# Kernel optimization log

Measured on AMD Instinct MI355X. Metric: run time of the kernel, lower is better.

Reference implementation:

```python
import jax, jax.numpy as jnp
from jax import lax
import numpy as np

B, IN, J, S, F, O, C, KS = 8, 8, 8, 187, 64, 64, 67, 15


def _ln(x, eps=1e-5):
    m = jnp.mean(x, axis=-1, keepdims=True)
    v = jnp.mean((x - m) ** 2, axis=-1, keepdims=True)
    return (x - m) / jnp.sqrt(v + eps)


def setup_inputs() -> dict:
    key = jax.random.key(0)
    ks = jax.random.split(key, 8)
    x_in = jax.random.normal(ks[0], (B, IN, S, F), jnp.float32)
    proj_x_prev = jax.random.normal(ks[1], (B, IN, S, O), jnp.float32)
    lin = jnp.linspace(-1.0, 1.0, C, dtype=jnp.float32)
    spline_weights = jnp.broadcast_to(lin, (IN, J, C)) + 0.01 * jax.random.normal(ks[2], (IN, J, C), jnp.float32)
    tau = 0.1 * jax.random.normal(ks[3], (IN, J), jnp.float32) + 0.1
    temperature = jnp.asarray(1.0, jnp.float32)
    omiga = jnp.full((IN, J), 0.2, jnp.float32)
    W2 = jax.random.normal(ks[4], (J, F, O), jnp.float32) * (1.0 / np.sqrt(F))
    b_param = 0.02 * jax.random.normal(ks[5], (J, S, O), jnp.float32)
    ln_scale = jnp.ones((J, F), jnp.float32)
    ln_bias = jnp.zeros((J, F), jnp.float32)
    alpha = jnp.ones((J,), jnp.float32)
    beta = jnp.ones((J,), jnp.float32)
    theta = jnp.ones((J,), jnp.float32)
    gamma = jnp.ones((J,), jnp.float32)
    w3 = 0.1 * jax.random.normal(ks[6], (J, O, KS), jnp.float32)  # depthwise conv kernels
    return dict(x_in=x_in, proj_x_prev=proj_x_prev, spline_weights=spline_weights, tau=tau,
                temperature=temperature, omiga=omiga, W2=W2, b_param=b_param, ln_scale=ln_scale,
                ln_bias=ln_bias, alpha=alpha, beta=beta, theta=theta, gamma=gamma, w3=w3)


def reference(x_in, proj_x_prev, spline_weights, tau, temperature, omiga, W2, b_param,
              ln_scale, ln_bias, alpha, beta, theta, gamma, w3):
    b, in_n, seq, feat = x_in.shape
    out_n, nC = spline_weights.shape[1], spline_weights.shape[2]
    kk = w3.shape[-1]
    # --- cubic B-spline basis ---
    h = 2.0 / (nC - 1)
    grid = jnp.linspace(-1.0, 1.0, nC, dtype=x_in.dtype)
    max_val = jnp.max(jnp.abs(x_in)) + 1e-8
    xn = jnp.clip(x_in / max_val * 0.95, -0.99, 0.99)
    dist = jnp.abs(xn[..., None] - grid) / h  # [b,in,seq,feat,C]
    basis = jax.nn.relu(2.0 - dist) ** 3 / 6.0 - jax.nn.relu(1.0 - dist) ** 3 * (4.0 / 6.0)
    spline_mapping = jnp.einsum('bisfc,ijc->bijsf', basis, spline_weights)
    activated = spline_mapping + jnp.abs(omiga)[None, :, :, None, None] * x_in[:, :, None]
    # --- energy-threshold gating ---
    energies = jnp.mean(activated ** 2, axis=(-1, -2))  # [b,in,out]
    tau_a = jnp.abs(tau)[None]
    t_val = jnp.abs(temperature) * np.sqrt(seq / 256.0) + 1e-4
    sqrtE = jnp.sqrt(energies + 1e-8)
    mask = jax.nn.sigmoid((sqrtE - tau_a) / t_val)  # [b,in,out]
    mult = sqrtE / (tau_a + 1e-8)
    wp = proj_x_prev[:, :, None] * (mult * mask)[..., None, None]  # [b,in,out,seq,d]
    d = wp.shape[-1]
    mid = in_n // 2
    Kt = wp[:, 0::2].transpose(0, 2, 3, 1, 4).reshape(b, out_n, seq, mid * d)
    Qt = wp[:, 1::2].transpose(0, 2, 3, 1, 4).reshape(b, out_n, seq, mid * d)
    Kt, Qt = _ln(Kt), _ln(Qt)
    raw = jnp.einsum('bjse,bjte->bjst', Kt, Qt)
    W1 = jax.nn.softmax(raw / (np.sqrt(mid * d) * t_val), axis=-1)  # [b,out,seq,seq]
    combined = jnp.einsum('bijsf,bij->bjsf', activated, mask)  # [b,out,seq,feat]
    # --- SplineWeightLayer (vectorized over out_n) ---
    xln = _ln(combined) * ln_scale[None, :, None, :] + ln_bias[None, :, None, :]
    x_prime = jnp.einsum('bjsh,jho->bjso', xln, W2) + b_param[None]  # [b,out,seq,O]
    o = x_prime.shape[-1]
    xt = x_prime.transpose(0, 2, 1, 3).reshape(b, seq, out_n * o)
    ker = w3.transpose(2, 0, 1).reshape(kk, 1, out_n * o)
    w3f = lax.conv_general_dilated(xt, ker, (1,), [(kk // 2, kk // 2)],
                                   dimension_numbers=('NWC', 'WIO', 'NWC'),
                                   feature_group_count=out_n * o)
    w3f = w3f.reshape(b, seq, out_n, o).transpose(0, 2, 1, 3)
    eye = jnp.eye(seq, dtype=x_in.dtype)
    attn_kernel = jnp.abs(beta)[None, :, None, None] * W1 + jnp.abs(alpha)[None, :, None, None] * eye
    global_part = jnp.einsum('bjst,bjto->bjso', attn_kernel, x_prime)
    spatial = global_part + jnp.abs(theta)[None, :, None, None] * w3f
    out = spatial + gamma[None, :, None, None] * combined  # residual_proj is Identity (F==O)
    return out, x_prime
```

## Files before the change

### kernel.cpp

```cpp
#include <hip/hip_runtime.h>
#include <math.h>

#define B_N 8
#define IN_N 8
#define J_N 8
#define S_N 187
#define F_N 64
#define O_N 64
#define C_N 67
#define KS_N 15
#define SF_N (S_N * F_N)
#define SF4_N (SF_N / 4)
#define E_N 256
#define SQRT_SF 0.85467470f

#define NT_SPL 12
#define NCOMB 96
#define NKTQT 2992
#define NZERO 16
#define NRAW 576
#define NXPR 768
#define NMAXP 256
#define FRAG_BJ 49152

typedef __attribute__((ext_vector_type(8))) _Float16 half8;
typedef __attribute__((ext_vector_type(4))) _Float16 half4;
typedef __attribute__((ext_vector_type(4))) float floatx4;

__device__ __forceinline__ float wave_sum(float v) {
#pragma unroll
  for (int off = 32; off > 0; off >>= 1) v += __shfl_down(v, off, 64);
  return __shfl(v, 0, 64);
}
__device__ __forceinline__ float wave_max(float v) {
#pragma unroll
  for (int off = 32; off > 0; off >>= 1) v = fmaxf(v, __shfl_down(v, off, 64));
  return __shfl(v, 0, 64);
}
__device__ __forceinline__ float lane_bc(float v, int l) {
  return __int_as_float(__builtin_amdgcn_readlane(__float_as_int(v), l));
}
__device__ __forceinline__ float bspline(float d) {
  float t2 = fmaxf(2.f - d, 0.f);
  float t1 = fmaxf(1.f - d, 0.f);
  return t2 * t2 * t2 * (1.f / 6.f) - t1 * t1 * t1 * (4.f / 6.f);
}
__device__ __forceinline__ float get_inv095(const float* __restrict__ maxp) {
  int lane = threadIdx.x & 63;
  float m = 0.f;
#pragma unroll
  for (int k = 0; k < NMAXP / 64; k++) m = fmaxf(m, maxp[lane + k * 64]);
  return 0.95f / (wave_max(m) + 1e-8f);
}
__device__ __forceinline__ float gate_g(const float* __restrict__ esum_p, int bi, int j,
                                        const float* __restrict__ tau, float tv) {
  const float* p = esum_p + ((long)bi * 8 + j) * NT_SPL;
  float s = 0.f;
#pragma unroll
  for (int k = 0; k < NT_SPL; k++) s += p[k];
  float sE = sqrtf(s * (1.f / (float)SF_N) + 1e-8f);
  float ta = fabsf(tau[(bi & 7) * 8 + j]);
  return (sE / (ta + 1e-8f)) / (1.f + expf(-(sE - ta) / tv));
}

__global__ void k_maxabs(const float4* __restrict__ x, float* __restrict__ maxp, int n4) {
  __shared__ float red[4];
  int tid = blockIdx.x * 256 + threadIdx.x;
  float m = 0.f;
  for (int i = tid; i < n4; i += gridDim.x * 256) {
    float4 v = x[i];
    m = fmaxf(m, fmaxf(fmaxf(fabsf(v.x), fabsf(v.y)), fmaxf(fabsf(v.z), fabsf(v.w))));
  }
  m = wave_max(m);
  if ((threadIdx.x & 63) == 0) red[threadIdx.x >> 6] = m;
  __syncthreads();
  if (threadIdx.x == 0)
    maxp[blockIdx.x] = fmaxf(fmaxf(red[0], red[1]), fmaxf(red[2], red[3]));
}

__global__ void k_spline(const float4* __restrict__ x4, const float* __restrict__ sw,
                         const float* __restrict__ omiga, const float* __restrict__ maxp,
                         float4* __restrict__ act4, float* __restrict__ esum_p) {
  int tile = blockIdx.x, bi = blockIdx.y;
  int i = bi & 7;
  __shared__ float wl[J_N * C_N];
  __shared__ float aom[J_N];
  __shared__ float red[4 * J_N];
  for (int t = threadIdx.x; t < J_N * C_N; t += 256) wl[t] = sw[i * J_N * C_N + t];
  if (threadIdx.x < J_N) aom[threadIdx.x] = fabsf(omiga[i * J_N + threadIdx.x]);
  int lane = threadIdx.x & 63, wid = threadIdx.x >> 6;
  float inv = get_inv095(maxp);
  __syncthreads();
  int i4 = tile * 256 + threadIdx.x;
  float e[J_N] = {0, 0, 0, 0, 0, 0, 0, 0};
  if (i4 < SF4_N) {
    float4 xv = x4[(long)bi * SF4_N + i4];
    float xs[4] = {xv.x, xv.y, xv.z, xv.w};
    float4 av[J_N];
#pragma unroll
    for (int c = 0; c < 4; c++) {
      float x = xs[c];
      float xn = fminf(fmaxf(x * inv, -0.99f), 0.99f);
      float u = (xn + 1.f) * 33.f;
      int c0 = (int)floorf(u) - 1;
      float sm[J_N] = {0, 0, 0, 0, 0, 0, 0, 0};
#pragma unroll
      for (int kk = 0; kk < 4; kk++) {
        int cc = c0 + kk;
        if (cc >= 0 && cc < C_N) {
          float bas = bspline(fabsf(u - (float)cc));
#pragma unroll
          for (int j = 0; j < J_N; j++) sm[j] += bas * wl[j * C_N + cc];
        }
      }
#pragma unroll
      for (int j = 0; j < J_N; j++) {
        float a = sm[j] + aom[j] * x;
        (&av[j].x)[c] = a;
        e[j] += a * a;
      }
    }
#pragma unroll
    for (int j = 0; j < J_N; j++) act4[((long)(bi * 8 + j)) * SF4_N + i4] = av[j];
  }
#pragma unroll
  for (int j = 0; j < J_N; j++) {
    float v = e[j];
#pragma unroll
    for (int off = 32; off > 0; off >>= 1) v += __shfl_down(v, off, 64);
    if (lane == 0) red[wid * J_N + j] = v;
  }
  __syncthreads();
  if (threadIdx.x < J_N)
    esum_p[((long)bi * 8 + threadIdx.x) * NT_SPL + tile] =
        red[threadIdx.x] + red[8 + threadIdx.x] + red[16 + threadIdx.x] + red[24 + threadIdx.x];
}

__global__ void k_mid2(const float4* __restrict__ act4, const float* __restrict__ esum_p,
                       const float* __restrict__ tau, const float* __restrict__ temp,
                       const float* __restrict__ proj, float4* __restrict__ comb4,
                       _Float16* __restrict__ khi, _Float16* __restrict__ klo,
                       _Float16* __restrict__ qhi, _Float16* __restrict__ qlo) {
  __shared__ float mk[64];
  int lane = threadIdx.x & 63;
  if (blockIdx.x < NCOMB) {
    int b = blockIdx.x / NT_SPL, tile = blockIdx.x - b * NT_SPL;
    if (threadIdx.x < 64) {
      int i = threadIdx.x >> 3, j = threadIdx.x & 7;
      const float* p = esum_p + ((long)(b * 8 + i) * 8 + j) * NT_SPL;
      float s = 0.f;
#pragma unroll
      for (int k = 0; k < NT_SPL; k++) s += p[k];
      float sE = sqrtf(s * (1.f / (float)SF_N) + 1e-8f);
      float ta = fabsf(tau[i * 8 + j]);
      float tv = fabsf(temp[0]) * SQRT_SF + 1e-4f;
      mk[threadIdx.x] = 1.f / (1.f + expf(-(sE - ta) / tv));
    }
    __syncthreads();
    int i4 = tile * 256 + threadIdx.x;
    if (i4 < SF4_N) {
      float4 cb[J_N] = {};
#pragma unroll
      for (int i = 0; i < IN_N; i++) {
#pragma unroll
        for (int j = 0; j < J_N; j++) {
          float4 a = act4[((long)((b * 8 + i) * 8 + j)) * SF4_N + i4];
          float g = mk[i * 8 + j];
          cb[j].x += g * a.x; cb[j].y += g * a.y;
          cb[j].z += g * a.z; cb[j].w += g * a.w;
        }
      }
#pragma unroll
      for (int j = 0; j < J_N; j++) comb4[((long)(b * J_N + j)) * SF4_N + i4] = cb[j];
    }
  } else if (blockIdx.x < NCOMB + NKTQT) {
    int w = threadIdx.x >> 6;
    int gr = (blockIdx.x - NCOMB) * 4 + w;
    int bj = gr / S_N, s = gr - bj * S_N;
    int b = bj >> 3, j = bj & 7;
    int ig = lane >> 4;
    int f4 = (lane & 15) * 4;
    int iK = b * 8 + 2 * ig;
    int iQ = iK + 1;
    float tv = fabsf(temp[0]) * SQRT_SF + 1e-4f;
    float gK = gate_g(esum_p, iK, j, tau, tv);
    float gQ = gate_g(esum_p, iQ, j, tau, tv);
    float4 kr = *(const float4*)(proj + ((long)iK * S_N + s) * 64 + f4);
    float4 qr = *(const float4*)(proj + ((long)iQ * S_N + s) * 64 + f4);
    float kv[4] = {kr.x * gK, kr.y * gK, kr.z * gK, kr.w * gK};
    float qv[4] = {qr.x * gQ, qr.y * gQ, qr.z * gQ, qr.w * gQ};
    float mkv = wave_sum(kv[0] + kv[1] + kv[2] + kv[3]) * (1.f / 256.f);
    float mqv = wave_sum(qv[0] + qv[1] + qv[2] + qv[3]) * (1.f / 256.f);
    float vk = 0.f, vq = 0.f;
#pragma unroll
    for (int q = 0; q < 4; q++) {
      float dk = kv[q] - mkv; vk += dk * dk;
      float dq = qv[q] - mqv; vq += dq * dq;
    }
    vk = wave_sum(vk) * (1.f / 256.f);
    vq = wave_sum(vq) * (1.f / 256.f);
    float ik = 1.f / sqrtf(vk + 1e-5f);
    float iq = 1.f / sqrtf(vq + 1e-5f);
    half4 hk4, lk4, hq4, lq4;
#pragma unroll
    for (int q = 0; q < 4; q++) {
      float fk = (kv[q] - mkv) * ik;
      float fq = (qv[q] - mqv) * iq;
      _Float16 hk = (_Float16)fk;
      _Float16 hq = (_Float16)fq;
      hk4[q] = hk; lk4[q] = (_Float16)(fk - (float)hk);
      hq4[q] = hq; lq4[q] = (_Float16)(fq - (float)hq);
    }
    int stile = s >> 4, m16 = s & 15;
    long fo = ((long)bj * 12 + stile) * 4096 + (lane >> 3) * 512 +
              (((lane >> 1) & 3) * 16 + m16) * 8 + (lane & 1) * 4;
    *(half4*)(khi + fo) = hk4;
    *(half4*)(klo + fo) = lk4;
    *(half4*)(qhi + fo) = hq4;
    *(half4*)(qlo + fo) = lq4;
  } else {
    int zb = blockIdx.x - (NCOMB + NKTQT);
    float4 z = {0.f, 0.f, 0.f, 0.f};
    for (int t = zb * 256 + threadIdx.x; t < 10240; t += NZERO * 256) {
      int bj = t / 160, r = t - bj * 160;
      int ec = r / 20, rr = r - ec * 20;
      int quad = rr / 5, m16 = 11 + rr - quad * 5;
      long fo = ((long)bj * 12 + 11) * 4096 + ec * 512 + (quad * 16 + m16) * 8;
      *(float4*)(khi + fo) = z;
      *(float4*)(klo + fo) = z;
      *(float4*)(qhi + fo) = z;
      *(float4*)(qlo + fo) = z;
    }
  }
}

__global__ void k_gemm(const _Float16* __restrict__ khi, const _Float16* __restrict__ klo,
                       const _Float16* __restrict__ qhi, const _Float16* __restrict__ qlo,
                       const float* __restrict__ temp, float* __restrict__ w1,
                       const float* __restrict__ comb, const float* __restrict__ W2,
                       const float* __restrict__ bparam, const float* __restrict__ lns,
                       const float* __restrict__ lnb, float* __restrict__ xprime) {
  __shared__ float smem[64 * 64 + 128];
  int lane = threadIdx.x & 63;
  if (blockIdx.x < NRAW) {
    int idx = blockIdx.x;
    int st = idx % 3, tt = (idx / 3) % 3, bj = idx / 9;
    int wave = threadIdx.x >> 6;
    int quad = lane >> 4, m16 = lane & 15;
    long fb = (long)bj * FRAG_BJ + lane * 8;
    const _Float16* ah_p = khi + fb + (st * 4 + wave) * 4096;
    const _Float16* al_p = klo + fb + (st * 4 + wave) * 4096;
    const _Float16* bh_p = qhi + fb + tt * 4 * 4096;
    const _Float16* bl_p = qlo + fb + tt * 4 * 4096;
    floatx4 acc[4] = {};
    for (int ec = 0; ec < 8; ec++) {
      half8 ah = *(const half8*)(ah_p + ec * 512);
      half8 al = *(const half8*)(al_p + ec * 512);
#pragma unroll
      for (int n = 0; n < 4; n++) {
        half8 bh = *(const half8*)(bh_p + n * 4096 + ec * 512);
        half8 bl = *(const half8*)(bl_p + n * 4096 + ec * 512);
        acc[n] = __builtin_amdgcn_mfma_f32_16x16x32_f16(ah, bh, acc[n], 0, 0, 0);
        acc[n] = __builtin_amdgcn_mfma_f32_16x16x32_f16(al, bh, acc[n], 0, 0, 0);
        acc[n] = __builtin_amdgcn_mfma_f32_16x16x32_f16(ah, bl, acc[n], 0, 0, 0);
      }
    }
    float tv = fabsf(temp[0]) * SQRT_SF + 1e-4f;
    float scale = 1.f / (16.f * tv);
#pragma unroll
    for (int n = 0; n < 4; n++) {
      int t = tt * 64 + n * 16 + m16;
      if (t >= S_N) continue;
#pragma unroll
      for (int r = 0; r < 4; r++) {
        int s = st * 64 + wave * 16 + quad * 4 + r;
        if (s < S_N) w1[((long)bj * S_N + s) * S_N + t] = acc[n][r] * scale;
      }
    }
  } else {
    int q = blockIdx.x - NRAW;
    int tile = q % 12, bj = q / 12;
    int j = bj & 7;
    float* w2s = smem;
    float* lss = smem + 4096;
    float* lbs = smem + 4160;
    const float4* wg = (const float4*)(W2 + j * 4096);
    float4* ws4 = (float4*)w2s;
    for (int idx = threadIdx.x; idx < 1024; idx += 256) ws4[idx] = wg[idx];
    if (threadIdx.x < 64) {
      lss[threadIdx.x] = lns[j * 64 + threadIdx.x];
      lbs[threadIdx.x] = lnb[j * 64 + threadIdx.x];
    }
    __syncthreads();
    int w = threadIdx.x >> 6;
    int sbase = tile * 16 + w * 4;
    float xln[4], acc[4];
#pragma unroll
    for (int rr = 0; rr < 4; rr++) {
      int s = sbase + rr;
      int sc = (s < S_N) ? s : S_N - 1;
      float x = comb[((long)bj * S_N + sc) * 64 + lane];
      float m = wave_sum(x) * (1.f / 64.f);
      float d = x - m;
      float var = wave_sum(d * d) * (1.f / 64.f);
      xln[rr] = d / sqrtf(var + 1e-5f) * lss[lane] + lbs[lane];
      acc[rr] = bparam[(j * S_N + sc) * 64 + lane];
    }
#pragma unroll
    for (int h = 0; h < 64; h++) {
      float w2v = w2s[h * 64 + lane];
#pragma unroll
      for (int rr = 0; rr < 4; rr++) acc[rr] += lane_bc(xln[rr], h) * w2v;
    }
#pragma unroll
    for (int rr = 0; rr < 4; rr++) {
      int s = sbase + rr;
      if (s < S_N) xprime[((long)bj * S_N + s) * 64 + lane] = acc[rr];
    }
  }
}

__global__ void k_final(const float* __restrict__ xprime, const float* __restrict__ w1,
                        const float* __restrict__ comb, const float* __restrict__ w3,
                        const float* __restrict__ alpha, const float* __restrict__ beta,
                        const float* __restrict__ theta, const float* __restrict__ gamma,
                        float* __restrict__ out) {
  int tile = blockIdx.x, bj = blockIdx.y;
  int j = bj & 7;
  __shared__ float w1t[16 * 188];
  int s0 = tile * 16;
  for (int idx = threadIdx.x; idx < 16 * S_N; idx += 256) {
    int r = idx / S_N, t = idx - r * S_N;
    int srow = s0 + r;
    w1t[r * 188 + t] = (srow < S_N) ? w1[((long)bj * S_N + srow) * S_N + t] : 0.f;
  }
  __syncthreads();
  int w = threadIdx.x >> 6, o = threadIdx.x & 63;
#pragma unroll
  for (int rr = 0; rr < 4; rr++) {
    float* row = &w1t[(w * 4 + rr) * 188];
    float v[3];
    float m = -1e30f;
#pragma unroll
    for (int q = 0; q < 3; q++) {
      int t = o + q * 64;
      v[q] = (t < S_N) ? row[t] : -1e30f;
      m = fmaxf(m, v[q]);
    }
    m = wave_max(m);
    float ssum = 0.f;
#pragma unroll
    for (int q = 0; q < 3; q++) {
      int t = o + q * 64;
      float e = (t < S_N) ? expf(v[q] - m) : 0.f;
      v[q] = e;
      ssum += e;
    }
    ssum = wave_sum(ssum);
    float invs = 1.f / ssum;
#pragma unroll
    for (int q = 0; q < 3; q++) {
      int t = o + q * 64;
      if (t < S_N) row[t] = v[q] * invs;
    }
  }
  float w3c[KS_N];
#pragma unroll
  for (int k = 0; k < KS_N; k++) w3c[k] = w3[j * 64 * KS_N + o * KS_N + k];
  const float* xpg = xprime + (long)bj * (S_N * 64);
  float aa = fabsf(alpha[j]), ba = fabsf(beta[j]), ta = fabsf(theta[j]), gv = gamma[j];
  float acc[4] = {0.f, 0.f, 0.f, 0.f};
  for (int t = 0; t < 184; t += 4) {
    float x0 = xpg[t * 64 + o];
    float x1 = xpg[(t + 1) * 64 + o];
    float x2 = xpg[(t + 2) * 64 + o];
    float x3 = xpg[(t + 3) * 64 + o];
#pragma unroll
    for (int rr = 0; rr < 4; rr++) {
      float4 wv = *(const float4*)&w1t[(w * 4 + rr) * 188 + t];
      acc[rr] += wv.x * x0 + wv.y * x1 + wv.z * x2 + wv.w * x3;
    }
  }
#pragma unroll
  for (int t = 184; t < S_N; t++) {
    float xv = xpg[t * 64 + o];
#pragma unroll
    for (int rr = 0; rr < 4; rr++) acc[rr] += w1t[(w * 4 + rr) * 188 + t] * xv;
  }
#pragma unroll
  for (int rr = 0; rr < 4; rr++) {
    int s = s0 + w * 4 + rr;
    if (s >= S_N) continue;
    float conv = 0.f;
#pragma unroll
    for (int k = 0; k < KS_N; k++) {
      int si = s + k - 7;
      if (si >= 0 && si < S_N) conv += xpg[si * 64 + o] * w3c[k];
    }
    float res = ba * acc[rr] + aa * xpg[s * 64 + o] + ta * conv +
                gv * comb[((long)bj * S_N + s) * 64 + o];
    out[((long)bj * S_N + s) * 64 + o] = res;
  }
}

extern "C" void kernel_launch(void* const* d_in, const int* in_sizes, int n_in,
                              void* d_out, int out_size, void* d_ws, size_t ws_size,
                              hipStream_t stream) {
  const float* x_in   = (const float*)d_in[0];
  const float* proj   = (const float*)d_in[1];
  const float* sw     = (const float*)d_in[2];
  const float* tau    = (const float*)d_in[3];
  const float* temp   = (const float*)d_in[4];
  const float* omiga  = (const float*)d_in[5];
  const float* W2     = (const float*)d_in[6];
  const float* bparam = (const float*)d_in[7];
  const float* lns    = (const float*)d_in[8];
  const float* lnb    = (const float*)d_in[9];
  const float* alpha  = (const float*)d_in[10];
  const float* beta   = (const float*)d_in[11];
  const float* theta  = (const float*)d_in[12];
  const float* gamma  = (const float*)d_in[13];
  const float* w3     = (const float*)d_in[14];

  float* out = (float*)d_out;
  float* xprime = out + B_N * J_N * S_N * O_N;

  float* wsf = (float*)d_ws;
  float* maxp   = wsf;
  float* esum_p = wsf + 512;
  float* act    = wsf + 512 + 512 * NT_SPL;
  const long FR = (long)64 * FRAG_BJ;
  _Float16* khi = (_Float16*)(act + (long)64 * 8 * SF_N);
  _Float16* klo = khi + FR;
  _Float16* qhi = klo + FR;
  _Float16* qlo = qhi + FR;
  float* w1   = (float*)(qlo + FR);
  float* comb = w1 + (long)B_N * J_N * S_N * S_N;

  k_maxabs<<<NMAXP, 256, 0, stream>>>((const float4*)x_in, maxp, (B_N * IN_N * S_N * F_N) / 4);
  k_spline<<<dim3(NT_SPL, 64), 256, 0, stream>>>((const float4*)x_in, sw, omiga, maxp,
                                                 (float4*)act, esum_p);
  k_mid2<<<NCOMB + NKTQT + NZERO, 256, 0, stream>>>((const float4*)act, esum_p, tau, temp,
                                                    proj, (float4*)comb, khi, klo, qhi, qlo);
  k_gemm<<<NRAW + NXPR, 256, 0, stream>>>(khi, klo, qhi, qlo, temp, w1,
                                          comb, W2, bparam, lns, lnb, xprime);
  k_final<<<dim3(12, 64), 256, 0, stream>>>(xprime, w1, comb, w3, alpha, beta, theta, gamma, out);
}
```

Baseline: 165.3 us.

## Recompute spline activations in combine stage instead of storing intermediate tensor

The spline kernel now computes only per-(b,i,j) energy sums and no longer writes the large activation tensor. The combine blocks of the middle kernel re-evaluate the B-spline basis from x_in for all input channels, then apply the gate mask directly. This trades a large global write and read of intermediates for duplicated spline arithmetic and a larger shared weight table in every block of the middle kernel.

Measured after the change: 169.4 us. 2.5% more time.

```diff
diff --git a/kernel.cpp b/kernel.cpp
--- a/kernel.cpp
+++ b/kernel.cpp
@@ -11,7 +11,6 @@
 #define KS_N 15
 #define SF_N (S_N * F_N)
 #define SF4_N (SF_N / 4)
-#define E_N 256
 #define SQRT_SF 0.85467470f
 
 #define NT_SPL 12
@@ -78,9 +77,9 @@
     maxp[blockIdx.x] = fmaxf(fmaxf(red[0], red[1]), fmaxf(red[2], red[3]));
 }
 
-__global__ void k_spline(const float4* __restrict__ x4, const float* __restrict__ sw,
-                         const float* __restrict__ omiga, const float* __restrict__ maxp,
-                         float4* __restrict__ act4, float* __restrict__ esum_p) {
+__global__ void k_energy2(const float4* __restrict__ x4, const float* __restrict__ sw,
+                          const float* __restrict__ omiga, const float* __restrict__ maxp,
+                          float* __restrict__ esum_p) {
   int tile = blockIdx.x, bi = blockIdx.y;
   int i = bi & 7;
   __shared__ float wl[J_N * C_N];
@@ -96,7 +95,6 @@
   if (i4 < SF4_N) {
     float4 xv = x4[(long)bi * SF4_N + i4];
     float xs[4] = {xv.x, xv.y, xv.z, xv.w};
-    float4 av[J_N];
 #pragma unroll
     for (int c = 0; c < 4; c++) {
       float x = xs[c];
@@ -116,12 +114,9 @@
 #pragma unroll
       for (int j = 0; j < J_N; j++) {
         float a = sm[j] + aom[j] * x;
-        (&av[j].x)[c] = a;
         e[j] += a * a;
       }
     }
-#pragma unroll
-    for (int j = 0; j < J_N; j++) act4[((long)(bi * 8 + j)) * SF4_N + i4] = av[j];
   }
 #pragma unroll
   for (int j = 0; j < J_N; j++) {
@@ -136,17 +131,23 @@
         red[threadIdx.x] + red[8 + threadIdx.x] + red[16 + threadIdx.x] + red[24 + threadIdx.x];
 }
 
-__global__ void k_mid2(const float4* __restrict__ act4, const float* __restrict__ esum_p,
-                       const float* __restrict__ tau, const float* __restrict__ temp,
-                       const float* __restrict__ proj, float4* __restrict__ comb4,
+__global__ void k_mid3(const float4* __restrict__ x4, const float* __restrict__ sw,
+                       const float* __restrict__ omiga, const float* __restrict__ maxp,
+                       const float* __restrict__ esum_p, const float* __restrict__ tau,
+                       const float* __restrict__ temp, const float* __restrict__ proj,
+                       float4* __restrict__ comb4,
                        _Float16* __restrict__ khi, _Float16* __restrict__ klo,
                        _Float16* __restrict__ qhi, _Float16* __restrict__ qlo) {
+  __shared__ float wl[IN_N * J_N * C_N];
+  __shared__ float aom[64];
   __shared__ float mk[64];
   int lane = threadIdx.x & 63;
   if (blockIdx.x < NCOMB) {
     int b = blockIdx.x / NT_SPL, tile = blockIdx.x - b * NT_SPL;
+    for (int t = threadIdx.x; t < IN_N * J_N * C_N; t += 256) wl[t] = sw[t];
     if (threadIdx.x < 64) {
       int i = threadIdx.x >> 3, j = threadIdx.x & 7;
+      aom[threadIdx.x] = fabsf(omiga[threadIdx.x]);
       const float* p = esum_p + ((long)(b * 8 + i) * 8 + j) * NT_SPL;
       float s = 0.f;
 #pragma unroll
@@ -156,18 +157,34 @@
       float tv = fabsf(temp[0]) * SQRT_SF + 1e-4f;
       mk[threadIdx.x] = 1.f / (1.f + expf(-(sE - ta) / tv));
     }
+    float inv = get_inv095(maxp);
     __syncthreads();
     int i4 = tile * 256 + threadIdx.x;
     if (i4 < SF4_N) {
       float4 cb[J_N] = {};
-#pragma unroll
       for (int i = 0; i < IN_N; i++) {
-#pragma unroll
-        for (int j = 0; j < J_N; j++) {
-          float4 a = act4[((long)((b * 8 + i) * 8 + j)) * SF4_N + i4];
-          float g = mk[i * 8 + j];
-          cb[j].x += g * a.x; cb[j].y += g * a.y;
-          cb[j].z += g * a.z; cb[j].w += g * a.w;
+        float4 xv = x4[((long)(b * 8 + i)) * SF4_N + i4];
+        float xs[4] = {xv.x, xv.y, xv.z, xv.w};
+#pragma unroll
+        for (int c = 0; c < 4; c++) {
+          float x = xs[c];
+          float xn = fminf(fmaxf(x * inv, -0.99f), 0.99f);
+          float u = (xn + 1.f) * 33.f;
+          int c0 = (int)floorf(u) - 1;
+          float sm[J_N] = {0, 0, 0, 0, 0, 0, 0, 0};
+#pragma unroll
+          for (int kk = 0; kk < 4; kk++) {
+            int cc = c0 + kk;
+            if (cc >= 0 && cc < C_N) {
+              float bas = bspline(fabsf(u - (float)cc));
+              const float* wli = wl + i * (J_N * C_N) + cc;
+#pragma unroll
+              for (int j = 0; j < J_N; j++) sm[j] += bas * wli[j * C_N];
+            }
+          }
+#pragma unroll
+          for (int j = 0; j < J_N; j++)
+            (&cb[j].x)[c] += (sm[j] + aom[i * 8 + j] * x) * mk[i * 8 + j];
         }
       }
 #pragma unroll
@@ -428,9 +445,8 @@
   float* wsf = (float*)d_ws;
   float* maxp   = wsf;
   float* esum_p = wsf + 512;
-  float* act    = wsf + 512 + 512 * NT_SPL;
   const long FR = (long)64 * FRAG_BJ;
-  _Float16* khi = (_Float16*)(act + (long)64 * 8 * SF_N);
+  _Float16* khi = (_Float16*)(wsf + 512 + 512 * NT_SPL);
   _Float16* klo = khi + FR;
   _Float16* qhi = klo + FR;
   _Float16* qlo = qhi + FR;
@@ -438,10 +454,10 @@
   float* comb = w1 + (long)B_N * J_N * S_N * S_N;
 
   k_maxabs<<<NMAXP, 256, 0, stream>>>((const float4*)x_in, maxp, (B_N * IN_N * S_N * F_N) / 4);
-  k_spline<<<dim3(NT_SPL, 64), 256, 0, stream>>>((const float4*)x_in, sw, omiga, maxp,
-                                                 (float4*)act, esum_p);
-  k_mid2<<<NCOMB + NKTQT + NZERO, 256, 0, stream>>>((const float4*)act, esum_p, tau, temp,
-                                                    proj, (float4*)comb, khi, klo, qhi, qlo);
+  k_energy2<<<dim3(NT_SPL, 64), 256, 0, stream>>>((const float4*)x_in, sw, omiga, maxp, esum_p);
+  k_mid3<<<NCOMB + NKTQT + NZERO, 256, 0, stream>>>((const float4*)x_in, sw, omiga, maxp,
+                                                    esum_p, tau, temp, proj, (float4*)comb,
+                                                    khi, klo, qhi, qlo);
   k_gemm<<<NRAW + NXPR, 256, 0, stream>>>(khi, klo, qhi, qlo, temp, w1,
                                           comb, W2, bparam, lns, lnb, xprime);
   k_final<<<dim3(12, 64), 256, 0, stream>>>(xprime, w1, comb, w3, alpha, beta, theta, gamma, out);
```

## Fuse attention logits GEMM into softmax-final kernel and stage K/Q fragments via LDS

Applied to the files above, without the earlier changes.

The MFMA logits GEMM moves into the final kernel, so each block computes a 48-row slab of W1 directly into shared memory, applies the softmax and the attention matmul there, and the global W1 buffer round trip goes away. The K/Q normalisation now handles a 16-row tile per block, staging fp16 hi/lo fragments in LDS and writing them out as coalesced float4 stores. This also zero-fills the padding rows, so the separate zeroing blocks are removed. The trade-off is that the final kernel now has only 256 blocks, each holding about 36KB of LDS and doing more serial work, which lowers parallelism.

After: 181.4 us. 1.1x slower.

```diff
diff --git a/kernel.cpp b/kernel.cpp
--- a/kernel.cpp
+++ b/kernel.cpp
@@ -11,14 +11,11 @@
 #define KS_N 15
 #define SF_N (S_N * F_N)
 #define SF4_N (SF_N / 4)
-#define E_N 256
 #define SQRT_SF 0.85467470f
 
 #define NT_SPL 12
 #define NCOMB 96
-#define NKTQT 2992
-#define NZERO 16
-#define NRAW 576
+#define NKT16 768
 #define NXPR 768
 #define NMAXP 256
 #define FRAG_BJ 49152
@@ -141,6 +138,7 @@
                        const float* __restrict__ proj, float4* __restrict__ comb4,
                        _Float16* __restrict__ khi, _Float16* __restrict__ klo,
                        _Float16* __restrict__ qhi, _Float16* __restrict__ qlo) {
+  __shared__ _Float16 stg[4][4096];
   __shared__ float mk[64];
   int lane = threadIdx.x & 63;
   if (blockIdx.x < NCOMB) {
@@ -173,172 +171,169 @@
 #pragma unroll
       for (int j = 0; j < J_N; j++) comb4[((long)(b * J_N + j)) * SF4_N + i4] = cb[j];
     }
-  } else if (blockIdx.x < NCOMB + NKTQT) {
+  } else {
+    int blk = blockIdx.x - NCOMB;
+    int bj = blk / 12, stile = blk - bj * 12;
+    int b = bj >> 3, j = bj & 7;
     int w = threadIdx.x >> 6;
-    int gr = (blockIdx.x - NCOMB) * 4 + w;
-    int bj = gr / S_N, s = gr - bj * S_N;
-    int b = bj >> 3, j = bj & 7;
     int ig = lane >> 4;
     int f4 = (lane & 15) * 4;
-    int iK = b * 8 + 2 * ig;
-    int iQ = iK + 1;
+    int iK = b * 8 + 2 * ig, iQ = iK + 1;
     float tv = fabsf(temp[0]) * SQRT_SF + 1e-4f;
     float gK = gate_g(esum_p, iK, j, tau, tv);
     float gQ = gate_g(esum_p, iQ, j, tau, tv);
-    float4 kr = *(const float4*)(proj + ((long)iK * S_N + s) * 64 + f4);
-    float4 qr = *(const float4*)(proj + ((long)iQ * S_N + s) * 64 + f4);
-    float kv[4] = {kr.x * gK, kr.y * gK, kr.z * gK, kr.w * gK};
-    float qv[4] = {qr.x * gQ, qr.y * gQ, qr.z * gQ, qr.w * gQ};
-    float mkv = wave_sum(kv[0] + kv[1] + kv[2] + kv[3]) * (1.f / 256.f);
-    float mqv = wave_sum(qv[0] + qv[1] + qv[2] + qv[3]) * (1.f / 256.f);
-    float vk = 0.f, vq = 0.f;
-#pragma unroll
-    for (int q = 0; q < 4; q++) {
-      float dk = kv[q] - mkv; vk += dk * dk;
-      float dq = qv[q] - mqv; vq += dq * dq;
-    }
-    vk = wave_sum(vk) * (1.f / 256.f);
-    vq = wave_sum(vq) * (1.f / 256.f);
-    float ik = 1.f / sqrtf(vk + 1e-5f);
-    float iq = 1.f / sqrtf(vq + 1e-5f);
-    half4 hk4, lk4, hq4, lq4;
-#pragma unroll
-    for (int q = 0; q < 4; q++) {
-      float fk = (kv[q] - mkv) * ik;
-      float fq = (qv[q] - mqv) * iq;
-      _Float16 hk = (_Float16)fk;
-      _Float16 hq = (_Float16)fq;
-      hk4[q] = hk; lk4[q] = (_Float16)(fk - (float)hk);
-      hq4[q] = hq; lq4[q] = (_Float16)(fq - (float)hq);
-    }
-    int stile = s >> 4, m16 = s & 15;
-    long fo = ((long)bj * 12 + stile) * 4096 + (lane >> 3) * 512 +
-              (((lane >> 1) & 3) * 16 + m16) * 8 + (lane & 1) * 4;
-    *(half4*)(khi + fo) = hk4;
-    *(half4*)(klo + fo) = lk4;
-    *(half4*)(qhi + fo) = hq4;
-    *(half4*)(qlo + fo) = lq4;
-  } else {
-    int zb = blockIdx.x - (NCOMB + NKTQT);
-    float4 z = {0.f, 0.f, 0.f, 0.f};
-    for (int t = zb * 256 + threadIdx.x; t < 10240; t += NZERO * 256) {
-      int bj = t / 160, r = t - bj * 160;
-      int ec = r / 20, rr = r - ec * 20;
-      int quad = rr / 5, m16 = 11 + rr - quad * 5;
-      long fo = ((long)bj * 12 + 11) * 4096 + ec * 512 + (quad * 16 + m16) * 8;
-      *(float4*)(khi + fo) = z;
-      *(float4*)(klo + fo) = z;
-      *(float4*)(qhi + fo) = z;
-      *(float4*)(qlo + fo) = z;
-    }
-  }
-}
-
-__global__ void k_gemm(const _Float16* __restrict__ khi, const _Float16* __restrict__ klo,
-                       const _Float16* __restrict__ qhi, const _Float16* __restrict__ qlo,
-                       const float* __restrict__ temp, float* __restrict__ w1,
-                       const float* __restrict__ comb, const float* __restrict__ W2,
-                       const float* __restrict__ bparam, const float* __restrict__ lns,
-                       const float* __restrict__ lnb, float* __restrict__ xprime) {
+    int slotbase = (lane >> 3) * 512 + ((lane >> 1) & 3) * 128 + (lane & 1) * 4;
+    for (int rr = 0; rr < 4; rr++) {
+      int m16 = w * 4 + rr;
+      int s = stile * 16 + m16;
+      half4 hk4 = {}, lk4 = {}, hq4 = {}, lq4 = {};
+      if (s < S_N) {
+        float4 kr = *(const float4*)(proj + ((long)iK * S_N + s) * 64 + f4);
+        float4 qr = *(const float4*)(proj + ((long)iQ * S_N + s) * 64 + f4);
+        float kv[4] = {kr.x * gK, kr.y * gK, kr.z * gK, kr.w * gK};
+        float qv[4] = {qr.x * gQ, qr.y * gQ, qr.z * gQ, qr.w * gQ};
+        float mkv = wave_sum(kv[0] + kv[1] + kv[2] + kv[3]) * (1.f / 256.f);
+        float mqv = wave_sum(qv[0] + qv[1] + qv[2] + qv[3]) * (1.f / 256.f);
+        float vk = 0.f, vq = 0.f;
+#pragma unroll
+        for (int q = 0; q < 4; q++) {
+          float dk = kv[q] - mkv; vk += dk * dk;
+          float dq = qv[q] - mqv; vq += dq * dq;
+        }
+        vk = wave_sum(vk) * (1.f / 256.f);
+        vq = wave_sum(vq) * (1.f / 256.f);
+        float ik = 1.f / sqrtf(vk + 1e-5f);
+        float iq = 1.f / sqrtf(vq + 1e-5f);
+#pragma unroll
+        for (int q = 0; q < 4; q++) {
+          float fk = (kv[q] - mkv) * ik;
+          float fq = (qv[q] - mqv) * iq;
+          _Float16 hk = (_Float16)fk;
+          _Float16 hq = (_Float16)fq;
+          hk4[q] = hk; lk4[q] = (_Float16)(fk - (float)hk);
+          hq4[q] = hq; lq4[q] = (_Float16)(fq - (float)hq);
+        }
+      }
+      int off = slotbase + m16 * 8;
+      *(half4*)&stg[0][off] = hk4;
+      *(half4*)&stg[1][off] = lk4;
+      *(half4*)&stg[2][off] = hq4;
+      *(half4*)&stg[3][off] = lq4;
+    }
+    __syncthreads();
+    long gb = ((long)bj * 12 + stile) * 4096;
+    float4* dk = (float4*)(khi + gb);
+    float4* dkl = (float4*)(klo + gb);
+    float4* dq = (float4*)(qhi + gb);
+    float4* dql = (float4*)(qlo + gb);
+    const float4* s0 = (const float4*)stg[0];
+    const float4* s1 = (const float4*)stg[1];
+    const float4* s2 = (const float4*)stg[2];
+    const float4* s3 = (const float4*)stg[3];
+    int t = threadIdx.x;
+    dk[t] = s0[t];  dk[t + 256] = s0[t + 256];
+    dkl[t] = s1[t]; dkl[t + 256] = s1[t + 256];
+    dq[t] = s2[t];  dq[t + 256] = s2[t + 256];
+    dql[t] = s3[t]; dql[t + 256] = s3[t + 256];
+  }
+}
+
+__global__ void k_xp(const float* __restrict__ comb, const float* __restrict__ W2,
+                     const float* __restrict__ bparam, const float* __restrict__ lns,
+                     const float* __restrict__ lnb, float* __restrict__ xprime) {
   __shared__ float smem[64 * 64 + 128];
   int lane = threadIdx.x & 63;
-  if (blockIdx.x < NRAW) {
-    int idx = blockIdx.x;
-    int st = idx % 3, tt = (idx / 3) % 3, bj = idx / 9;
-    int wave = threadIdx.x >> 6;
-    int quad = lane >> 4, m16 = lane & 15;
-    long fb = (long)bj * FRAG_BJ + lane * 8;
-    const _Float16* ah_p = khi + fb + (st * 4 + wave) * 4096;
-    const _Float16* al_p = klo + fb + (st * 4 + wave) * 4096;
-    const _Float16* bh_p = qhi + fb + tt * 4 * 4096;
-    const _Float16* bl_p = qlo + fb + tt * 4 * 4096;
-    floatx4 acc[4] = {};
+  int tile = blockIdx.x % 12, bj = blockIdx.x / 12;
+  int j = bj & 7;
+  float* w2s = smem;
+  float* lss = smem + 4096;
+  float* lbs = smem + 4160;
+  const float4* wg = (const float4*)(W2 + j * 4096);
+  float4* ws4 = (float4*)w2s;
+  for (int idx = threadIdx.x; idx < 1024; idx += 256) ws4[idx] = wg[idx];
+  if (threadIdx.x < 64) {
+    lss[threadIdx.x] = lns[j * 64 + threadIdx.x];
+    lbs[threadIdx.x] = lnb[j * 64 + threadIdx.x];
+  }
+  __syncthreads();
+  int w = threadIdx.x >> 6;
+  int sbase = tile * 16 + w * 4;
+  float xln[4], acc[4];
+#pragma unroll
+  for (int rr = 0; rr < 4; rr++) {
+    int s = sbase + rr;
+    int sc = (s < S_N) ? s : S_N - 1;
+    float x = comb[((long)bj * S_N + sc) * 64 + lane];
+    float m = wave_sum(x) * (1.f / 64.f);
+    float d = x - m;
+    float var = wave_sum(d * d) * (1.f / 64.f);
+    xln[rr] = d / sqrtf(var + 1e-5f) * lss[lane] + lbs[lane];
+    acc[rr] = bparam[(j * S_N + sc) * 64 + lane];
+  }
+#pragma unroll
+  for (int h = 0; h < 64; h++) {
+    float w2v = w2s[h * 64 + lane];
+#pragma unroll
+    for (int rr = 0; rr < 4; rr++) acc[rr] += lane_bc(xln[rr], h) * w2v;
+  }
+#pragma unroll
+  for (int rr = 0; rr < 4; rr++) {
+    int s = sbase + rr;
+    if (s < S_N) xprime[((long)bj * S_N + s) * 64 + lane] = acc[rr];
+  }
+}
+
+__global__ void k_rawfinal(const _Float16* __restrict__ khi, const _Float16* __restrict__ klo,
+                           const _Float16* __restrict__ qhi, const _Float16* __restrict__ qlo,
+                           const float* __restrict__ temp, const float* __restrict__ xprime,
+                           const float* __restrict__ comb, const float* __restrict__ w3,
+                           const float* __restrict__ alpha, const float* __restrict__ beta,
+                           const float* __restrict__ theta, const float* __restrict__ gamma,
+                           float* __restrict__ out) {
+  __shared__ float w1t[48 * 188];
+  int chunk = blockIdx.x, bj = blockIdx.y;
+  int j = bj & 7;
+  int w = threadIdx.x >> 6, lane = threadIdx.x & 63;
+  int quad = lane >> 4, m16 = lane & 15;
+  long fb = (long)bj * FRAG_BJ + lane * 8;
+  floatx4 acc[3][3] = {};
+#pragma unroll
+  for (int ts = 0; ts < 3; ts++) {
+    const _Float16* ah_p = khi + fb + (long)(chunk * 3 + ts) * 4096;
+    const _Float16* al_p = klo + fb + (long)(chunk * 3 + ts) * 4096;
     for (int ec = 0; ec < 8; ec++) {
       half8 ah = *(const half8*)(ah_p + ec * 512);
       half8 al = *(const half8*)(al_p + ec * 512);
 #pragma unroll
-      for (int n = 0; n < 4; n++) {
-        half8 bh = *(const half8*)(bh_p + n * 4096 + ec * 512);
-        half8 bl = *(const half8*)(bl_p + n * 4096 + ec * 512);
-        acc[n] = __builtin_amdgcn_mfma_f32_16x16x32_f16(ah, bh, acc[n], 0, 0, 0);
-        acc[n] = __builtin_amdgcn_mfma_f32_16x16x32_f16(al, bh, acc[n], 0, 0, 0);
-        acc[n] = __builtin_amdgcn_mfma_f32_16x16x32_f16(ah, bl, acc[n], 0, 0, 0);
-      }
-    }
-    float tv = fabsf(temp[0]) * SQRT_SF + 1e-4f;
-    float scale = 1.f / (16.f * tv);
-#pragma unroll
-    for (int n = 0; n < 4; n++) {
-      int t = tt * 64 + n * 16 + m16;
+      for (int n = 0; n < 3; n++) {
+        long bo = fb + (long)(w * 3 + n) * 4096 + ec * 512;
+        half8 bh = *(const half8*)(qhi + bo);
+        half8 bl = *(const half8*)(qlo + bo);
+        acc[ts][n] = __builtin_amdgcn_mfma_f32_16x16x32_f16(ah, bh, acc[ts][n], 0, 0, 0);
+        acc[ts][n] = __builtin_amdgcn_mfma_f32_16x16x32_f16(al, bh, acc[ts][n], 0, 0, 0);
+        acc[ts][n] = __builtin_amdgcn_mfma_f32_16x16x32_f16(ah, bl, acc[ts][n], 0, 0, 0);
+      }
+    }
+  }
+  float tv = fabsf(temp[0]) * SQRT_SF + 1e-4f;
+  float scale = 1.f / (16.f * tv);
+#pragma unroll
+  for (int ts = 0; ts < 3; ts++)
+#pragma unroll
+    for (int n = 0; n < 3; n++) {
+      int t = (w * 3 + n) * 16 + m16;
       if (t >= S_N) continue;
 #pragma unroll
-      for (int r = 0; r < 4; r++) {
-        int s = st * 64 + wave * 16 + quad * 4 + r;
-        if (s < S_N) w1[((long)bj * S_N + s) * S_N + t] = acc[n][r] * scale;
-      }
-    }
-  } else {
-    int q = blockIdx.x - NRAW;
-    int tile = q % 12, bj = q / 12;
-    int j = bj & 7;
-    float* w2s = smem;
-    float* lss = smem + 4096;
-    float* lbs = smem + 4160;
-    const float4* wg = (const float4*)(W2 + j * 4096);
-    float4* ws4 = (float4*)w2s;
-    for (int idx = threadIdx.x; idx < 1024; idx += 256) ws4[idx] = wg[idx];
-    if (threadIdx.x < 64) {
-      lss[threadIdx.x] = lns[j * 64 + threadIdx.x];
-      lbs[threadIdx.x] = lnb[j * 64 + threadIdx.x];
-    }
-    __syncthreads();
-    int w = threadIdx.x >> 6;
-    int sbase = tile * 16 + w * 4;
-    float xln[4], acc[4];
-#pragma unroll
-    for (int rr = 0; rr < 4; rr++) {
-      int s = sbase + rr;
-      int sc = (s < S_N) ? s : S_N - 1;
-      float x = comb[((long)bj * S_N + sc) * 64 + lane];
-      float m = wave_sum(x) * (1.f / 64.f);
-      float d = x - m;
-      float var = wave_sum(d * d) * (1.f / 64.f);
-      xln[rr] = d / sqrtf(var + 1e-5f) * lss[lane] + lbs[lane];
-      acc[rr] = bparam[(j * S_N + sc) * 64 + lane];
-    }
-#pragma unroll
-    for (int h = 0; h < 64; h++) {
-      float w2v = w2s[h * 64 + lane];
-#pragma unroll
-      for (int rr = 0; rr < 4; rr++) acc[rr] += lane_bc(xln[rr], h) * w2v;
-    }
-#pragma unroll
-    for (int rr = 0; rr < 4; rr++) {
-      int s = sbase + rr;
-      if (s < S_N) xprime[((long)bj * S_N + s) * 64 + lane] = acc[rr];
-    }
-  }
-}
-
-__global__ void k_final(const float* __restrict__ xprime, const float* __restrict__ w1,
-                        const float* __restrict__ comb, const float* __restrict__ w3,
-                        const float* __restrict__ alpha, const float* __restrict__ beta,
-                        const float* __restrict__ theta, const float* __restrict__ gamma,
-                        float* __restrict__ out) {
-  int tile = blockIdx.x, bj = blockIdx.y;
-  int j = bj & 7;
-  __shared__ float w1t[16 * 188];
-  int s0 = tile * 16;
-  for (int idx = threadIdx.x; idx < 16 * S_N; idx += 256) {
-    int r = idx / S_N, t = idx - r * S_N;
-    int srow = s0 + r;
-    w1t[r * 188 + t] = (srow < S_N) ? w1[((long)bj * S_N + srow) * S_N + t] : 0.f;
-  }
-  __syncthreads();
-  int w = threadIdx.x >> 6, o = threadIdx.x & 63;
-#pragma unroll
-  for (int rr = 0; rr < 4; rr++) {
-    float* row = &w1t[(w * 4 + rr) * 188];
+      for (int r = 0; r < 4; r++)
+        w1t[(ts * 16 + quad * 4 + r) * 188 + t] = acc[ts][n][r] * scale;
+    }
+  __syncthreads();
+  int o = lane;
+#pragma unroll
+  for (int rr = 0; rr < 12; rr++) {
+    int rl = w * 12 + rr;
+    if (chunk * 48 + rl >= S_N) continue;
+    float* row = &w1t[rl * 188];
     float v[3];
     float m = -1e30f;
 #pragma unroll
@@ -364,42 +359,46 @@
       if (t < S_N) row[t] = v[q] * invs;
     }
   }
+  __syncthreads();
   float w3c[KS_N];
 #pragma unroll
   for (int k = 0; k < KS_N; k++) w3c[k] = w3[j * 64 * KS_N + o * KS_N + k];
   const float* xpg = xprime + (long)bj * (S_N * 64);
   float aa = fabsf(alpha[j]), ba = fabsf(beta[j]), ta = fabsf(theta[j]), gv = gamma[j];
-  float acc[4] = {0.f, 0.f, 0.f, 0.f};
-  for (int t = 0; t < 184; t += 4) {
-    float x0 = xpg[t * 64 + o];
-    float x1 = xpg[(t + 1) * 64 + o];
-    float x2 = xpg[(t + 2) * 64 + o];
-    float x3 = xpg[(t + 3) * 64 + o];
+  for (int g = 0; g < 3; g++) {
+    int rbase = w * 12 + g * 4;
+    float acc2[4] = {0.f, 0.f, 0.f, 0.f};
+    for (int t = 0; t < 184; t += 4) {
+      float x0 = xpg[t * 64 + o];
+      float x1 = xpg[(t + 1) * 64 + o];
+      float x2 = xpg[(t + 2) * 64 + o];
+      float x3 = xpg[(t + 3) * 64 + o];
+#pragma unroll
+      for (int rr = 0; rr < 4; rr++) {
+        float4 wv = *(const float4*)&w1t[(rbase + rr) * 188 + t];
+        acc2[rr] += wv.x * x0 + wv.y * x1 + wv.z * x2 + wv.w * x3;
+      }
+    }
+#pragma unroll
+    for (int t = 184; t < S_N; t++) {
+      float xv = xpg[t * 64 + o];
+#pragma unroll
+      for (int rr = 0; rr < 4; rr++) acc2[rr] += w1t[(rbase + rr) * 188 + t] * xv;
+    }
 #pragma unroll
     for (int rr = 0; rr < 4; rr++) {
-      float4 wv = *(const float4*)&w1t[(w * 4 + rr) * 188 + t];
-      acc[rr] += wv.x * x0 + wv.y * x1 + wv.z * x2 + wv.w * x3;
-    }
-  }
-#pragma unroll
-  for (int t = 184; t < S_N; t++) {
-    float xv = xpg[t * 64 + o];
-#pragma unroll
-    for (int rr = 0; rr < 4; rr++) acc[rr] += w1t[(w * 4 + rr) * 188 + t] * xv;
-  }
-#pragma unroll
-  for (int rr = 0; rr < 4; rr++) {
-    int s = s0 + w * 4 + rr;
-    if (s >= S_N) continue;
-    float conv = 0.f;
-#pragma unroll
-    for (int k = 0; k < KS_N; k++) {
-      int si = s + k - 7;
-      if (si >= 0 && si < S_N) conv += xpg[si * 64 + o] * w3c[k];
-    }
-    float res = ba * acc[rr] + aa * xpg[s * 64 + o] + ta * conv +
-                gv * comb[((long)bj * S_N + s) * 64 + o];
-    out[((long)bj * S_N + s) * 64 + o] = res;
+      int s = chunk * 48 + rbase + rr;
+      if (s >= S_N) continue;
+      float conv = 0.f;
+#pragma unroll
+      for (int k = 0; k < KS_N; k++) {
+        int si = s + k - 7;
+        if (si >= 0 && si < S_N) conv += xpg[si * 64 + o] * w3c[k];
+      }
+      float res = ba * acc2[rr] + aa * xpg[s * 64 + o] + ta * conv +
+                  gv * comb[((long)bj * S_N + s) * 64 + o];
+      out[((long)bj * S_N + s) * 64 + o] = res;
+    }
   }
 }
 
@@ -429,20 +428,20 @@
   float* maxp   = wsf;
   float* esum_p = wsf + 512;
   float* act    = wsf + 512 + 512 * NT_SPL;
+  const long ACT_N = (long)64 * 8 * SF_N;
   const long FR = (long)64 * FRAG_BJ;
-  _Float16* khi = (_Float16*)(act + (long)64 * 8 * SF_N);
+  _Float16* khi = (_Float16*)(act + ACT_N);
   _Float16* klo = khi + FR;
   _Float16* qhi = klo + FR;
   _Float16* qlo = qhi + FR;
-  float* w1   = (float*)(qlo + FR);
-  float* comb = w1 + (long)B_N * J_N * S_N * S_N;
+  float* comb = (float*)(qlo + FR);
 
   k_maxabs<<<NMAXP, 256, 0, stream>>>((const float4*)x_in, maxp, (B_N * IN_N * S_N * F_N) / 4);
   k_spline<<<dim3(NT_SPL, 64), 256, 0, stream>>>((const float4*)x_in, sw, omiga, maxp,
                                                  (float4*)act, esum_p);
-  k_mid2<<<NCOMB + NKTQT + NZERO, 256, 0, stream>>>((const float4*)act, esum_p, tau, temp,
-                                                    proj, (float4*)comb, khi, klo, qhi, qlo);
-  k_gemm<<<NRAW + NXPR, 256, 0, stream>>>(khi, klo, qhi, qlo, temp, w1,
-                                          comb, W2, bparam, lns, lnb, xprime);
-  k_final<<<dim3(12, 64), 256, 0, stream>>>(xprime, w1, comb, w3, alpha, beta, theta, gamma, out);
-}
+  k_mid2<<<NCOMB + NKT16, 256, 0, stream>>>((const float4*)act, esum_p, tau, temp,
+                                            proj, (float4*)comb, khi, klo, qhi, qlo);
+  k_xp<<<NXPR, 256, 0, stream>>>(comb, W2, bparam, lns, lnb, xprime);
+  k_rawfinal<<<dim3(4, 64), 256, 0, stream>>>(khi, klo, qhi, qlo, temp, xprime, comb,
+                                              w3, alpha, beta, theta, gamma, out);
+}
```

## Split combine over j-pairs and stage K/Q fragment tiles in LDS for coalesced stores

Applied to the files above, without the earlier changes.

The combine part of k_mid2 now uses 384 blocks, each handling two output channels instead of all eight. This cuts per-thread register accumulators and raises parallelism. The K/Q normalisation part now gives each block a full 16-row s-tile: each wave handles four rows and writes the fp16 hi/lo fragments into shared memory, then the block writes them out as contiguous float4 stores. Rows past the end are zero-filled, which replaces the separate zeroing blocks. The cost is 32KB of LDS per block, which may limit occupancy, plus an extra barrier.

New measurement: 165.6 us. No clear change (+0.2%).

```diff
diff --git a/kernel.cpp b/kernel.cpp
--- a/kernel.cpp
+++ b/kernel.cpp
@@ -11,13 +11,11 @@
 #define KS_N 15
 #define SF_N (S_N * F_N)
 #define SF4_N (SF_N / 4)
-#define E_N 256
 #define SQRT_SF 0.85467470f
 
 #define NT_SPL 12
-#define NCOMB 96
-#define NKTQT 2992
-#define NZERO 16
+#define NCOMB 384
+#define NKT16 768
 #define NRAW 576
 #define NXPR 768
 #define NMAXP 256
@@ -141,12 +139,16 @@
                        const float* __restrict__ proj, float4* __restrict__ comb4,
                        _Float16* __restrict__ khi, _Float16* __restrict__ klo,
                        _Float16* __restrict__ qhi, _Float16* __restrict__ qlo) {
-  __shared__ float mk[64];
+  __shared__ _Float16 stg[4][4096];
+  __shared__ float mk[16];
   int lane = threadIdx.x & 63;
   if (blockIdx.x < NCOMB) {
-    int b = blockIdx.x / NT_SPL, tile = blockIdx.x - b * NT_SPL;
-    if (threadIdx.x < 64) {
-      int i = threadIdx.x >> 3, j = threadIdx.x & 7;
+    int blk = blockIdx.x;
+    int tile = blk % 12, bjg = blk / 12;
+    int jg = bjg & 3, b = bjg >> 2;
+    int j0 = jg * 2;
+    if (threadIdx.x < 16) {
+      int i = threadIdx.x >> 1, j = j0 + (threadIdx.x & 1);
       const float* p = esum_p + ((long)(b * 8 + i) * 8 + j) * NT_SPL;
       float s = 0.f;
 #pragma unroll
@@ -159,78 +161,85 @@
     __syncthreads();
     int i4 = tile * 256 + threadIdx.x;
     if (i4 < SF4_N) {
-      float4 cb[J_N] = {};
+      float4 cb[2] = {};
 #pragma unroll
       for (int i = 0; i < IN_N; i++) {
 #pragma unroll
-        for (int j = 0; j < J_N; j++) {
-          float4 a = act4[((long)((b * 8 + i) * 8 + j)) * SF4_N + i4];
-          float g = mk[i * 8 + j];
-          cb[j].x += g * a.x; cb[j].y += g * a.y;
-          cb[j].z += g * a.z; cb[j].w += g * a.w;
+        for (int jj = 0; jj < 2; jj++) {
+          float4 a = act4[((long)((b * 8 + i) * 8 + j0 + jj)) * SF4_N + i4];
+          float g = mk[i * 2 + jj];
+          cb[jj].x += g * a.x; cb[jj].y += g * a.y;
+          cb[jj].z += g * a.z; cb[jj].w += g * a.w;
         }
       }
 #pragma unroll
-      for (int j = 0; j < J_N; j++) comb4[((long)(b * J_N + j)) * SF4_N + i4] = cb[j];
-    }
-  } else if (blockIdx.x < NCOMB + NKTQT) {
+      for (int jj = 0; jj < 2; jj++)
+        comb4[((long)(b * J_N + j0 + jj)) * SF4_N + i4] = cb[jj];
+    }
+  } else {
+    int blk = blockIdx.x - NCOMB;
+    int bj = blk / 12, stile = blk - bj * 12;
+    int b = bj >> 3, j = bj & 7;
     int w = threadIdx.x >> 6;
-    int gr = (blockIdx.x - NCOMB) * 4 + w;
-    int bj = gr / S_N, s = gr - bj * S_N;
-    int b = bj >> 3, j = bj & 7;
     int ig = lane >> 4;
     int f4 = (lane & 15) * 4;
-    int iK = b * 8 + 2 * ig;
-    int iQ = iK + 1;
+    int iK = b * 8 + 2 * ig, iQ = iK + 1;
     float tv = fabsf(temp[0]) * SQRT_SF + 1e-4f;
     float gK = gate_g(esum_p, iK, j, tau, tv);
     float gQ = gate_g(esum_p, iQ, j, tau, tv);
-    float4 kr = *(const float4*)(proj + ((long)iK * S_N + s) * 64 + f4);
-    float4 qr = *(const float4*)(proj + ((long)iQ * S_N + s) * 64 + f4);
-    float kv[4] = {kr.x * gK, kr.y * gK, kr.z * gK, kr.w * gK};
-    float qv[4] = {qr.x * gQ, qr.y * gQ, qr.z * gQ, qr.w * gQ};
-    float mkv = wave_sum(kv[0] + kv[1] + kv[2] + kv[3]) * (1.f / 256.f);
-    float mqv = wave_sum(qv[0] + qv[1] + qv[2] + qv[3]) * (1.f / 256.f);
-    float vk = 0.f, vq = 0.f;
-#pragma unroll
-    for (int q = 0; q < 4; q++) {
-      float dk = kv[q] - mkv; vk += dk * dk;
-      float dq = qv[q] - mqv; vq += dq * dq;
-    }
-    vk = wave_sum(vk) * (1.f / 256.f);
-    vq = wave_sum(vq) * (1.f / 256.f);
-    float ik = 1.f / sqrtf(vk + 1e-5f);
-    float iq = 1.f / sqrtf(vq + 1e-5f);
-    half4 hk4, lk4, hq4, lq4;
-#pragma unroll
-    for (int q = 0; q < 4; q++) {
-      float fk = (kv[q] - mkv) * ik;
-      float fq = (qv[q] - mqv) * iq;
-      _Float16 hk = (_Float16)fk;
-      _Float16 hq = (_Float16)fq;
-      hk4[q] = hk; lk4[q] = (_Float16)(fk - (float)hk);
-      hq4[q] = hq; lq4[q] = (_Float16)(fq - (float)hq);
-    }
-    int stile = s >> 4, m16 = s & 15;
-    long fo = ((long)bj * 12 + stile) * 4096 + (lane >> 3) * 512 +
-              (((lane >> 1) & 3) * 16 + m16) * 8 + (lane & 1) * 4;
-    *(half4*)(khi + fo) = hk4;
-    *(half4*)(klo + fo) = lk4;
-    *(half4*)(qhi + fo) = hq4;
-    *(half4*)(qlo + fo) = lq4;
-  } else {
-    int zb = blockIdx.x - (NCOMB + NKTQT);
-    float4 z = {0.f, 0.f, 0.f, 0.f};
-    for (int t = zb * 256 + threadIdx.x; t < 10240; t += NZERO * 256) {
-      int bj = t / 160, r = t - bj * 160;
-      int ec = r / 20, rr = r - ec * 20;
-      int quad = rr / 5, m16 = 11 + rr - quad * 5;
-      long fo = ((long)bj * 12 + 11) * 4096 + ec * 512 + (quad * 16 + m16) * 8;
-      *(float4*)(khi + fo) = z;
-      *(float4*)(klo + fo) = z;
-      *(float4*)(qhi + fo) = z;
-      *(float4*)(qlo + fo) = z;
-    }
+    int slotbase = (lane >> 3) * 512 + ((lane >> 1) & 3) * 128 + (lane & 1) * 4;
+    for (int rr = 0; rr < 4; rr++) {
+      int m16 = w * 4 + rr;
+      int s = stile * 16 + m16;
+      half4 hk4 = {}, lk4 = {}, hq4 = {}, lq4 = {};
+      if (s < S_N) {
+        float4 kr = *(const float4*)(proj + ((long)iK * S_N + s) * 64 + f4);
+        float4 qr = *(const float4*)(proj + ((long)iQ * S_N + s) * 64 + f4);
+        float kv[4] = {kr.x * gK, kr.y * gK, kr.z * gK, kr.w * gK};
+        float qv[4] = {qr.x * gQ, qr.y * gQ, qr.z * gQ, qr.w * gQ};
+        float mkv = wave_sum(kv[0] + kv[1] + kv[2] + kv[3]) * (1.f / 256.f);
+        float mqv = wave_sum(qv[0] + qv[1] + qv[2] + qv[3]) * (1.f / 256.f);
+        float vk = 0.f, vq = 0.f;
+#pragma unroll
+        for (int q = 0; q < 4; q++) {
+          float dk = kv[q] - mkv; vk += dk * dk;
+          float dq = qv[q] - mqv; vq += dq * dq;
+        }
+        vk = wave_sum(vk) * (1.f / 256.f);
+        vq = wave_sum(vq) * (1.f / 256.f);
+        float ik = 1.f / sqrtf(vk + 1e-5f);
+        float iq = 1.f / sqrtf(vq + 1e-5f);
+#pragma unroll
+        for (int q = 0; q < 4; q++) {
+          float fk = (kv[q] - mkv) * ik;
+          float fq = (qv[q] - mqv) * iq;
+          _Float16 hk = (_Float16)fk;
+          _Float16 hq = (_Float16)fq;
+          hk4[q] = hk; lk4[q] = (_Float16)(fk - (float)hk);
+          hq4[q] = hq; lq4[q] = (_Float16)(fq - (float)hq);
+        }
+      }
+      int off = slotbase + m16 * 8;
+      *(half4*)&stg[0][off] = hk4;
+      *(half4*)&stg[1][off] = lk4;
+      *(half4*)&stg[2][off] = hq4;
+      *(half4*)&stg[3][off] = lq4;
+    }
+    __syncthreads();
+    long gb = ((long)bj * 12 + stile) * 4096;
+    float4* dk = (float4*)(khi + gb);
+    float4* dkl = (float4*)(klo + gb);
+    float4* dq = (float4*)(qhi + gb);
+    float4* dql = (float4*)(qlo + gb);
+    const float4* s0 = (const float4*)stg[0];
+    const float4* s1 = (const float4*)stg[1];
+    const float4* s2 = (const float4*)stg[2];
+    const float4* s3 = (const float4*)stg[3];
+    int t = threadIdx.x;
+    dk[t] = s0[t];  dk[t + 256] = s0[t + 256];
+    dkl[t] = s1[t]; dkl[t + 256] = s1[t + 256];
+    dq[t] = s2[t];  dq[t + 256] = s2[t + 256];
+    dql[t] = s3[t]; dql[t + 256] = s3[t + 256];
   }
 }
 
@@ -429,8 +438,9 @@
   float* maxp   = wsf;
   float* esum_p = wsf + 512;
   float* act    = wsf + 512 + 512 * NT_SPL;
+  const long ACT_N = (long)64 * 8 * SF_N;
   const long FR = (long)64 * FRAG_BJ;
-  _Float16* khi = (_Float16*)(act + (long)64 * 8 * SF_N);
+  _Float16* khi = (_Float16*)(act + ACT_N);
   _Float16* klo = khi + FR;
   _Float16* qhi = klo + FR;
   _Float16* qlo = qhi + FR;
@@ -440,8 +450,8 @@
   k_maxabs<<<NMAXP, 256, 0, stream>>>((const float4*)x_in, maxp, (B_N * IN_N * S_N * F_N) / 4);
   k_spline<<<dim3(NT_SPL, 64), 256, 0, stream>>>((const float4*)x_in, sw, omiga, maxp,
                                                  (float4*)act, esum_p);
-  k_mid2<<<NCOMB + NKTQT + NZERO, 256, 0, stream>>>((const float4*)act, esum_p, tau, temp,
-                                                    proj, (float4*)comb, khi, klo, qhi, qlo);
+  k_mid2<<<NCOMB + NKT16, 256, 0, stream>>>((const float4*)act, esum_p, tau, temp,
+                                            proj, (float4*)comb, khi, klo, qhi, qlo);
   k_gemm<<<NRAW + NXPR, 256, 0, stream>>>(khi, klo, qhi, qlo, temp, w1,
                                           comb, W2, bparam, lns, lnb, xprime);
   k_final<<<dim3(12, 64), 256, 0, stream>>>(xprime, w1, comb, w3, alpha, beta, theta, gamma, out);
```
